# Kernel tuning notes

Hardware: AMD Instinct MI355X
Metric: run time of the kernel (lower is better)

The kernel has to match this reference:

```python
import jax, jax.numpy as jnp
import numpy as np
import math

B, L, LC = 2, 2048, 2048
D_MODEL, D_CROSS, D_HEAD = 1024, 1024, 64
N_HEADS = D_MODEL // D_HEAD
D6 = D_HEAD // 6  # freq bands per spatial axis (k-diffusion AxialRoPE, 3 axes)
EPS = 1e-6


def rope_freqs():
    n = N_HEADS * D6
    f = jnp.exp(jnp.linspace(math.log(math.pi), math.log(10.0 * math.pi), n + 1)[:-1])
    return f.reshape(D6, N_HEADS).T  # [nh, d6]


def rope_theta(pos):
    # pos: [b, l, 3] -> theta: [b, nh, l, 3*d6]
    f = rope_freqs()
    th = jnp.concatenate([pos[..., None, a:a + 1] * f for a in range(3)], axis=-1)  # [b,l,nh,3*d6]
    return jnp.moveaxis(th, -2, -3)


def apply_rotary(x, theta):
    d = theta.shape[-1]
    x1, x2, x3 = x[..., :d], x[..., d:2 * d], x[..., 2 * d:]
    c, s = jnp.cos(theta), jnp.sin(theta)
    return jnp.concatenate([x1 * c - x2 * s, x2 * c + x1 * s, x3], axis=-1)


def rms_norm(x, scale, eps=EPS):
    ms = jnp.mean(x * x, axis=-1, keepdims=True)
    return x * (scale * jax.lax.rsqrt(ms + eps))


def cosine_scale(q, k, scale, eps=EPS):
    s = jnp.sqrt(scale)[:, None, None]  # [nh,1,1]
    qn = q * (s * jax.lax.rsqrt(jnp.sum(q * q, axis=-1, keepdims=True) + eps))
    kn = k * (s * jax.lax.rsqrt(jnp.sum(k * k, axis=-1, keepdims=True) + eps))
    return qn, kn


def setup_inputs():
    key = jax.random.key(0)
    ks = jax.random.split(key, 8)
    return {
        "x": jax.random.normal(ks[0], (B, L, D_MODEL), jnp.float32),
        "pos": jax.random.uniform(ks[1], (B, L, 3), jnp.float32),
        "x_cross": jax.random.normal(ks[2], (B, LC, D_CROSS), jnp.float32),
        "pos_cross": jax.random.uniform(ks[3], (B, LC, 3), jnp.float32),
        "norm_scale": jnp.ones((D_MODEL,), jnp.float32),
        "norm_cross_scale": jnp.ones((D_CROSS,), jnp.float32),
        "q_w": jax.random.normal(ks[4], (D_MODEL, D_MODEL), jnp.float32) * 0.02,
        "kv_w": jax.random.normal(ks[5], (2 * D_MODEL, D_CROSS), jnp.float32) * 0.02,
        "head_scale": jnp.full((N_HEADS,), 10.0, jnp.float32),
        "out_w": jax.random.normal(ks[6], (D_MODEL, D_MODEL), jnp.float32) * 0.02,
    }


def reference(x, pos, x_cross, pos_cross, norm_scale, norm_cross_scale, q_w, kv_w, head_scale, out_w):
    skip = x
    xn = rms_norm(x, norm_scale)
    xc = rms_norm(x_cross, norm_cross_scale)
    q = xn @ q_w.T                       # [b,l,d]
    kv = xc @ kv_w.T                     # [b,lc,2d]
    b, l, _ = q.shape
    lc = kv.shape[1]
    q = q.reshape(b, l, N_HEADS, D_HEAD).transpose(0, 2, 1, 3)          # [b,nh,l,e]
    kv = kv.reshape(b, lc, 2, N_HEADS, D_HEAD)                          # (t nh e) factorization
    k = kv[:, :, 0].transpose(0, 2, 1, 3)
    v = kv[:, :, 1].transpose(0, 2, 1, 3)
    q, k = cosine_scale(q, k, head_scale)
    q = apply_rotary(q, rope_theta(pos))
    k = apply_rotary(k, rope_theta(pos_cross))
    attn = jax.nn.softmax(jnp.einsum('bhqe,bhke->bhqk', q, k), axis=-1)  # scale=1.0 (cosine-sim pre-scaled)
    o = jnp.einsum('bhqk,bhke->bhqe', attn, v)
    o = o.transpose(0, 2, 1, 3).reshape(b, l, D_MODEL)
    return o @ out_w.T + skip
```

## Files before the change

### kernel.cpp

```cpp
#include <hip/hip_runtime.h>

typedef __bf16 bf16_t;
typedef __bf16 bf16x4 __attribute__((ext_vector_type(4)));
typedef __bf16 bf16x8 __attribute__((ext_vector_type(8)));
typedef float f32x4 __attribute__((ext_vector_type(4)));
typedef short s16x4 __attribute__((ext_vector_type(4)));

#define B_DIM 2
#define L_DIM 2048
#define LC_DIM 2048
#define DM 1024
#define NH 16
#define DH 64
#define MB (1u << 20)
#define LOG2E 1.44269504088896f
#define NZ 2

__device__ __forceinline__ bool probe_is_f32(const unsigned* probe) {
  return probe[0] == 0x3F800000u;
}

__device__ __forceinline__ void async16(const bf16_t* g, bf16_t* l) {
  __builtin_amdgcn_global_load_lds((const __attribute__((address_space(1))) void*)g,
                                   (__attribute__((address_space(3))) void*)l, 16, 0, 0);
}

#if __has_builtin(__builtin_amdgcn_mfma_f32_16x16x16bf16_1k)
#define HAVE_K16 1
__device__ __forceinline__ f32x4 mfma16(bf16x4 a, bf16x4 b, f32x4 c) {
  union { bf16x4 h; s16x4 s; } ua, ub;
  ua.h = a; ub.h = b;
  return __builtin_amdgcn_mfma_f32_16x16x16bf16_1k(ua.s, ub.s, c, 0, 0, 0);
}
#else
#define HAVE_K16 0
#endif

__device__ __forceinline__ void conv_b(const void* src, bf16_t* dst, int i, bool f32) {
  bf16x4 w;
  if (f32) {
    f32x4 v = *(const f32x4*)((const float*)src + i);
    w[0] = (bf16_t)v[0]; w[1] = (bf16_t)v[1]; w[2] = (bf16_t)v[2]; w[3] = (bf16_t)v[3];
  } else {
    w = *(const bf16x4*)((const bf16_t*)src + i);
  }
  *(bf16x4*)(dst + i) = w;
}
__device__ __forceinline__ void conv_f(const void* src, float* dst, int i, int n, bool f32) {
  if (i >= n) return;
  f32x4 v;
  if (f32) {
    v = *(const f32x4*)((const float*)src + i);
  } else {
    bf16x4 w = *(const bf16x4*)((const bf16_t*)src + i);
    v[0] = (float)w[0]; v[1] = (float)w[1]; v[2] = (float)w[2]; v[3] = (float)w[3];
  }
  *(f32x4*)(dst + i) = v;
}

__global__ __launch_bounds__(256) void front_k(
    const void* x, const void* xc, const void* qw, const void* kvw, const void* ow,
    const void* pos, const void* posc, const void* ns, const void* ncs, const void* hs,
    bf16_t* xn, bf16_t* xcn, bf16_t* cqw, bf16_t* ckvw, bf16_t* cow,
    float* fpos, float* fposc, float* fns, float* fncs, float* fhs,
    const unsigned* probe) {
  const bool f32 = probe_is_f32(probe);
  const int tid = threadIdx.x;
  if (blockIdx.x < 2 * B_DIM * L_DIM) {
    const bool isB = blockIdx.x >= B_DIM * L_DIM;
    const int row = isB ? blockIdx.x - B_DIM * L_DIM : blockIdx.x;
    const void* src = isB ? xc : x;
    const void* scr = isB ? ncs : ns;
    bf16_t* out = isB ? xcn : xn;
    float f0, f1, f2, f3, s0, s1, s2, s3;
    if (f32) {
      f32x4 v = *((const f32x4*)((const float*)src + (size_t)row * DM) + tid);
      f0 = v[0]; f1 = v[1]; f2 = v[2]; f3 = v[3];
      f32x4 sv = *((const f32x4*)scr + tid);
      s0 = sv[0]; s1 = sv[1]; s2 = sv[2]; s3 = sv[3];
    } else {
      bf16x4 v = *((const bf16x4*)((const bf16_t*)src + (size_t)row * DM) + tid);
      f0 = (float)v[0]; f1 = (float)v[1]; f2 = (float)v[2]; f3 = (float)v[3];
      bf16x4 sv = *((const bf16x4*)scr + tid);
      s0 = (float)sv[0]; s1 = (float)sv[1]; s2 = (float)sv[2]; s3 = (float)sv[3];
    }
    float ss = f0 * f0 + f1 * f1 + f2 * f2 + f3 * f3;
#pragma unroll
    for (int m = 1; m < 64; m <<= 1) ss += __shfl_xor(ss, m, 64);
    __shared__ float red[4];
    const int wave = tid >> 6, lane = tid & 63;
    if (lane == 0) red[wave] = ss;
    __syncthreads();
    float ms = (red[0] + red[1] + red[2] + red[3]) * (1.0f / DM);
    float r = rsqrtf(ms + 1e-6f);
    bf16x4 w;
    w[0] = (bf16_t)(f0 * r * s0);
    w[1] = (bf16_t)(f1 * r * s1);
    w[2] = (bf16_t)(f2 * r * s2);
    w[3] = (bf16_t)(f3 * r * s3);
    *(bf16x4*)(out + (size_t)row * DM + tid * 4) = w;
    return;
  }
  const int blk = blockIdx.x - 2 * B_DIM * L_DIM;
  const int e4 = tid * 4;
  if (blk < 1024)       conv_b(qw,  cqw,  blk * 1024 + e4, f32);
  else if (blk < 3072)  conv_b(kvw, ckvw, (blk - 1024) * 1024 + e4, f32);
  else if (blk < 4096)  conv_b(ow,  cow,  (blk - 3072) * 1024 + e4, f32);
  else if (blk < 4108)  conv_f(pos,  fpos,  (blk - 4096) * 1024 + e4, 12288, f32);
  else if (blk < 4120)  conv_f(posc, fposc, (blk - 4108) * 1024 + e4, 12288, f32);
  else if (blk == 4120) conv_f(ns,  fns,  e4, 1024, f32);
  else if (blk == 4121) conv_f(ncs, fncs, e4, 1024, f32);
  else                  conv_f(hs,  fhs,  e4, 16, f32);
}

__global__ __launch_bounds__(256) void gemm_qkv_k(const bf16_t* __restrict__ xn,
                                                  const bf16_t* __restrict__ xcn,
                                                  const bf16_t* __restrict__ qw,
                                                  const bf16_t* __restrict__ kvw,
                                                  bf16_t* __restrict__ qb,
                                                  bf16_t* __restrict__ kvK,
                                                  bf16_t* __restrict__ Vp) {
  __shared__ bf16_t Asm[128 * 32];
  __shared__ bf16_t Wsm[128 * 32];
  const int tid = threadIdx.x;
  const int wave = tid >> 6, lane = tid & 63;
  const int quad = lane >> 4, tc = lane & 15;
  const int wr = wave >> 1, wc = wave & 1;
  const bool isq = blockIdx.y < 8;
  const bf16_t* A = isq ? xn : xcn;
  const bf16_t* W = isq ? qw : kvw;
  const int n0 = (isq ? blockIdx.y : (blockIdx.y - 8)) * 128;
  const int m0 = blockIdx.x * 128;
  const int K = 1024;

  const int srow = wave * 16 + (lane >> 2);
  const int scol = (lane & 3) * 8;
  const bf16_t* ag = A + (size_t)(m0 + srow) * K + scol;
  const bf16_t* wg = W + (size_t)(n0 + srow) * K + scol;
  bf16_t* al0 = &Asm[(wave * 16) * 32];
  bf16_t* al1 = &Asm[(64 + wave * 16) * 32];
  bf16_t* wl0 = &Wsm[(wave * 16) * 32];
  bf16_t* wl1 = &Wsm[(64 + wave * 16) * 32];

  f32x4 acc[4][4] = {};

  for (int k0 = 0; k0 < K; k0 += 32) {
    async16(ag + k0, al0);
    async16(ag + k0 + (size_t)64 * K, al1);
    async16(wg + k0, wl0);
    async16(wg + k0 + (size_t)64 * K, wl1);
    __syncthreads();
    bf16x8 af[4], wf[4];
#pragma unroll
    for (int i = 0; i < 4; ++i)
      af[i] = *(const bf16x8*)&Asm[(wr * 64 + i * 16 + tc) * 32 + quad * 8];
#pragma unroll
    for (int j = 0; j < 4; ++j)
      wf[j] = *(const bf16x8*)&Wsm[(wc * 64 + j * 16 + tc) * 32 + quad * 8];
#pragma unroll
    for (int i = 0; i < 4; ++i)
#pragma unroll
      for (int j = 0; j < 4; ++j)
        acc[i][j] = __builtin_amdgcn_mfma_f32_16x16x32_bf16(af[i], wf[j], acc[i][j], 0, 0, 0);
    __syncthreads();
  }

  if (isq || n0 < DM) {
    bf16_t* C = isq ? qb : kvK;
#pragma unroll
    for (int i = 0; i < 4; ++i) {
      const size_t row = (size_t)m0 + wr * 64 + i * 16 + quad * 4;
#pragma unroll
      for (int j = 0; j < 4; ++j) {
        const int col = n0 + wc * 64 + j * 16 + tc;
#pragma unroll
        for (int r = 0; r < 4; ++r)
          C[(row + r) * DM + col] = (bf16_t)acc[i][j][r];
      }
    }
  } else {
#pragma unroll
    for (int i = 0; i < 4; ++i) {
      const int row = m0 + wr * 64 + i * 16 + quad * 4;
      const int b = row >> 11, kc = row & (LC_DIM - 1);
#pragma unroll
      for (int j = 0; j < 4; ++j) {
        const int hd = n0 - DM + wc * 64 + j * 16 + tc;
        const int h = hd >> 6, d = hd & 63;
        bf16x4 pk;
        pk[0] = (bf16_t)acc[i][j][0];
        pk[1] = (bf16_t)acc[i][j][1];
        pk[2] = (bf16_t)acc[i][j][2];
        pk[3] = (bf16_t)acc[i][j][3];
        *(bf16x4*)(Vp + (((size_t)(b * NH + h) * (LC_DIM / 4) + (kc >> 2)) * DH + d) * 4) = pk;
      }
    }
  }
}

__global__ __launch_bounds__(256) void prep_k(bf16_t* __restrict__ q,
                                              const bf16_t* __restrict__ kvK,
                                              bf16_t* __restrict__ Kp,
                                              const float* __restrict__ pos,
                                              const float* __restrict__ pos_cross,
                                              const float* __restrict__ head_scale) {
  const int gw = (blockIdx.x * blockDim.x + threadIdx.x) >> 6;
  const int lane = threadIdx.x & 63;
  const int per = B_DIM * L_DIM * NH;
  const bool is_k = gw >= per;
  const int id = is_k ? gw - per : gw;
  const int h = id & 15;
  const int row = id >> 4;
  const bf16_t* src = (is_k ? kvK : q) + (size_t)row * DM + h * DH;
  const float* pp = (is_k ? pos_cross : pos) + (size_t)row * 3;

  float val = (float)src[lane];
  float ss = val * val;
#pragma unroll
  for (int m = 1; m < 64; m <<= 1) ss += __shfl_xor(ss, m, 64);
  float sc = sqrtf(head_scale[h]) * rsqrtf(ss + 1e-6f);
  if (!is_k) sc *= LOG2E;
  float vn = val * sc;

  const int j = lane;
  const int tj = j < 30 ? j : (j < 60 ? j - 30 : 0);
  const int a = tj >= 20 ? 2 : (tj >= 10 ? 1 : 0);
  const int jj = tj - a * 10;
  float p = pp[a];
  float freq = 3.14159265358979f *
               __builtin_amdgcn_exp2f((float)(jj * 16 + h) * 0.0207620505930f);
  float rev = p * freq * 0.15915494309189535f;
  rev -= floorf(rev);
  float cth = __builtin_amdgcn_cosf(rev);
  float sth = __builtin_amdgcn_sinf(rev);
  const int partner = j < 30 ? j + 30 : (j < 60 ? j - 30 : j);
  float vp = __shfl(vn, partner, 64);
  float outv;
  if (j < 30)       outv = vn * cth - vp * sth;
  else if (j < 60)  outv = vn * cth + vp * sth;
  else              outv = vn;

  if (is_k) {
    const int b = row >> 11, l = row & (LC_DIM - 1);
    Kp[(((size_t)b * NH + h) * LC_DIM + l) * DH + lane] = (bf16_t)outv;
  } else {
    q[(size_t)row * DM + h * DH + lane] = (bf16_t)outv;
  }
}

#define FLASH_LOAD(KB, VB, KC)                                                   \
  {                                                                              \
    _Pragma("unroll") for (int mt = 0; mt < 4; ++mt) {                           \
      _Pragma("unroll") for (int hf = 0; hf < 2; ++hf)                           \
        KB[mt][hf] = *(const bf16x8*)(kg + (size_t)((KC) + mt * 16 + tc) * DH +  \
                                      hf * 32 + quad * 8);                       \
      _Pragma("unroll") for (int dt = 0; dt < 4; ++dt)                           \
        VB[mt][dt] = *(const bf16x4*)(vp + ((size_t)(((KC) >> 2) + mt * 4 + quad) * DH + \
                                            dt * 16 + tc) * 4);                  \
    }                                                                            \
  }

#define FLASH_COMPUTE(KB, VB)                                                    \
  {                                                                              \
    _Pragma("unroll") for (int jj = 0; jj < 4; ++jj) {                           \
      f32x4 s[4];                                                                \
      _Pragma("unroll") for (int mt = 0; mt < 4; ++mt) {                         \
        f32x4 zf = {0.f, 0.f, 0.f, 0.f};                                         \
        zf = __builtin_amdgcn_mfma_f32_16x16x32_bf16(KB[mt][0], qf[jj][0], zf, 0, 0, 0); \
        zf = __builtin_amdgcn_mfma_f32_16x16x32_bf16(KB[mt][1], qf[jj][1], zf, 0, 0, 0); \
        s[mt] = zf;                                                              \
      }                                                                          \
      bf16x4 p[4];                                                               \
      _Pragma("unroll") for (int mt = 0; mt < 4; ++mt) {                         \
        p[mt][0] = (bf16_t)__builtin_amdgcn_exp2f(s[mt][0]);                     \
        p[mt][1] = (bf16_t)__builtin_amdgcn_exp2f(s[mt][1]);                     \
        p[mt][2] = (bf16_t)__builtin_amdgcn_exp2f(s[mt][2]);                     \
        p[mt][3] = (bf16_t)__builtin_amdgcn_exp2f(s[mt][3]);                     \
      }                                                                          \
      _Pragma("unroll") for (int mt = 0; mt < 4; ++mt) {                         \
        accL[jj] = mfma16(p[mt], ones, accL[jj]);                                \
        _Pragma("unroll") for (int dt = 0; dt < 4; ++dt)                         \
          accO[jj][dt] = mfma16(p[mt], VB[mt][dt], accO[jj][dt]);                \
      }                                                                          \
    }                                                                            \
  }

__global__ __launch_bounds__(64, 2) void flash12_k(const bf16_t* __restrict__ q,
                                                   const bf16_t* __restrict__ Kp,
                                                   const bf16_t* __restrict__ Vp,
                                                   bf16_t* __restrict__ Op,
                                                   float* __restrict__ lp) {
  const int lane = threadIdx.x;
  const int quad = lane >> 4, tc = lane & 15;
  const int bh = blockIdx.y, b = bh >> 4;
  const int z = blockIdx.z;
  const int q0 = blockIdx.x * 64;

  bf16x8 qf[4][2];
#pragma unroll
  for (int jj = 0; jj < 4; ++jj)
#pragma unroll
    for (int hf = 0; hf < 2; ++hf)
      qf[jj][hf] = *(const bf16x8*)(q + (size_t)(b * L_DIM + q0 + jj * 16 + tc) * DM +
                                    (bh & 15) * DH + hf * 32 + quad * 8);

  f32x4 accO[4][4] = {};
  const bf16_t* kg = Kp + (size_t)bh * LC_DIM * DH;
  const bf16_t* vp = Vp + (size_t)bh * (LC_DIM / 4) * DH * 4;
  const int base = z * 1024;

#if HAVE_K16
  f32x4 accL[4] = {};
  bf16x4 ones;
  ones[0] = (bf16_t)1.0f; ones[1] = (bf16_t)1.0f;
  ones[2] = (bf16_t)1.0f; ones[3] = (bf16_t)1.0f;

  bf16x8 k0f[4][2], k1f[4][2];
  bf16x4 v0f[4][4], v1f[4][4];
  FLASH_LOAD(k0f, v0f, base);
#pragma unroll 1
  for (int kc0 = base; kc0 < base + 1024; kc0 += 128) {
    FLASH_LOAD(k1f, v1f, kc0 + 64);
    FLASH_COMPUTE(k0f, v0f);
    if (kc0 + 128 < base + 1024) FLASH_LOAD(k0f, v0f, kc0 + 128);
    FLASH_COMPUTE(k1f, v1f);
  }
#else
  __shared__ bf16_t Psm[64 * 64];
  float lsum[4] = {0.f, 0.f, 0.f, 0.f};
  const int sw = tc & 7;
#pragma unroll 1
  for (int kc0 = base; kc0 < base + 1024; kc0 += 64) {
    bf16x8 kfr[4][2];
#pragma unroll
    for (int mt = 0; mt < 4; ++mt)
#pragma unroll
      for (int hf = 0; hf < 2; ++hf)
        kfr[mt][hf] = *(const bf16x8*)(kg + (size_t)(kc0 + mt * 16 + tc) * DH +
                                       hf * 32 + quad * 8);
#pragma unroll
    for (int jj = 0; jj < 4; ++jj) {
      f32x4 s[4];
#pragma unroll
      for (int mt = 0; mt < 4; ++mt) {
        f32x4 zf = {0.f, 0.f, 0.f, 0.f};
        zf = __builtin_amdgcn_mfma_f32_16x16x32_bf16(kfr[mt][0], qf[jj][0], zf, 0, 0, 0);
        zf = __builtin_amdgcn_mfma_f32_16x16x32_bf16(kfr[mt][1], qf[jj][1], zf, 0, 0, 0);
        s[mt] = zf;
      }
#pragma unroll
      for (int mt = 0; mt < 4; ++mt) {
        float p0 = __builtin_amdgcn_exp2f(s[mt][0]);
        float p1 = __builtin_amdgcn_exp2f(s[mt][1]);
        float p2 = __builtin_amdgcn_exp2f(s[mt][2]);
        float p3 = __builtin_amdgcn_exp2f(s[mt][3]);
        lsum[jj] += (p0 + p1) + (p2 + p3);
        bf16x4 pk;
        pk[0] = (bf16_t)p0; pk[1] = (bf16_t)p1; pk[2] = (bf16_t)p2; pk[3] = (bf16_t)p3;
        const int phys = (mt * 2 + (quad >> 1)) ^ sw;
        *(bf16x4*)&Psm[(jj * 16 + tc) * 64 + phys * 8 + (quad & 1) * 4] = pk;
      }
    }
#pragma unroll
    for (int kb = 0; kb < 2; ++kb) {
      bf16x8 vfull[4];
#pragma unroll
      for (int dt = 0; dt < 4; ++dt) {
        const size_t k4 = (size_t)((kc0 + kb * 32) >> 2) + quad * 2;
        bf16x4 lo = *(const bf16x4*)(vp + (k4 * DH + dt * 16 + tc) * 4);
        bf16x4 hi = *(const bf16x4*)(vp + ((k4 + 1) * DH + dt * 16 + tc) * 4);
#pragma unroll
        for (int e = 0; e < 4; ++e) { vfull[dt][e] = lo[e]; vfull[dt][4 + e] = hi[e]; }
      }
#pragma unroll
      for (int jp = 0; jp < 4; ++jp) {
        bf16x8 pf = *(const bf16x8*)&Psm[(jp * 16 + tc) * 64 + ((kb * 4 + quad) ^ sw) * 8];
#pragma unroll
        for (int dt = 0; dt < 4; ++dt)
          accO[jp][dt] = __builtin_amdgcn_mfma_f32_16x16x32_bf16(pf, vfull[dt], accO[jp][dt], 0, 0, 0);
      }
    }
  }
#endif

  bf16_t* Ob = Op + (size_t)(z * 32 + bh) * L_DIM * DH;
  float* lb = lp + (size_t)(z * 32 + bh) * L_DIM;
#if HAVE_K16
#pragma unroll
  for (int jj = 0; jj < 4; ++jj) {
    if (tc == 0) {
#pragma unroll
      for (int r = 0; r < 4; ++r) lb[q0 + jj * 16 + quad * 4 + r] = accL[jj][r];
    }
#pragma unroll
    for (int r = 0; r < 4; ++r) {
      const size_t qg = q0 + jj * 16 + quad * 4 + r;
#pragma unroll
      for (int dt = 0; dt < 4; ++dt)
        Ob[qg * DH + dt * 16 + tc] = (bf16_t)accO[jj][dt][r];
    }
  }
#else
#pragma unroll
  for (int jj = 0; jj < 4; ++jj) {
    lsum[jj] += __shfl_xor(lsum[jj], 16, 64);
    lsum[jj] += __shfl_xor(lsum[jj], 32, 64);
  }
#pragma unroll
  for (int jj = 0; jj < 4; ++jj) {
    if (quad == 0) lb[q0 + jj * 16 + tc] = lsum[jj];
#pragma unroll
    for (int r = 0; r < 4; ++r) {
      const size_t qg = q0 + jj * 16 + quad * 4 + r;
#pragma unroll
      for (int dt = 0; dt < 4; ++dt)
        Ob[qg * DH + dt * 16 + tc] = (bf16_t)accO[jj][dt][r];
    }
  }
#endif
}

__global__ __launch_bounds__(256) void gemm_out_k(const bf16_t* __restrict__ Op,
                                                  const float* __restrict__ lp,
                                                  const bf16_t* __restrict__ W,
                                                  const void* __restrict__ skip_raw,
                                                  void* __restrict__ out,
                                                  const unsigned* __restrict__ probe) {
  __shared__ bf16_t Asm[64 * 32];
  __shared__ bf16_t Wsm[128 * 32];
  const int tid = threadIdx.x;
  const int wave = tid >> 6, lane = tid & 63;
  const int quad = lane >> 4, tc = lane & 15;
  const int wr = wave >> 1, wc = wave & 1;
  const int m0 = blockIdx.x * 64, n0 = blockIdx.y * 128;
  const int K = 1024, N = 1024;

  const int srow = wave * 16 + (lane >> 2);
  const int scol = (lane & 3) * 8;
  const int arow = m0 + srow;
  const int bb = arow >> 11, l = arow & (L_DIM - 1);
  const size_t zoff = (size_t)32 * L_DIM * DH;
  const bf16_t* wg = W + (size_t)(n0 + srow) * K + scol;
  bf16_t* wl0 = &Wsm[(wave * 16) * 32];
  bf16_t* wl1 = &Wsm[(64 + wave * 16) * 32];

  f32x4 acc[2][4] = {};

  float lv0 = lp[(size_t)(bb * NH) * L_DIM + l];
  float lv1 = lp[(size_t)(32 + bb * NH) * L_DIM + l];
  bf16x8 a0 = *(const bf16x8*)(Op + ((size_t)(bb * NH) * L_DIM + l) * DH + scol);
  bf16x8 a1 = *(const bf16x8*)(Op + zoff + ((size_t)(bb * NH) * L_DIM + l) * DH + scol);

  for (int k0 = 0; k0 < K; k0 += 32) {
    async16(wg + k0, wl0);
    async16(wg + k0 + (size_t)64 * K, wl1);
    const float linv = 1.f / (lv0 + lv1);
    bf16x8 aw;
#pragma unroll
    for (int e = 0; e < 8; ++e)
      aw[e] = (bf16_t)(((float)a0[e] + (float)a1[e]) * linv);
    *(bf16x8*)&Asm[srow * 32 + scol] = aw;
    if (k0 + 32 < K) {
      const int kn = k0 + 32;
      const int bhn = bb * NH + (kn >> 6);
      if ((kn & 63) == 0) {
        lv0 = lp[(size_t)bhn * L_DIM + l];
        lv1 = lp[(size_t)(32 + bhn) * L_DIM + l];
      }
      const size_t obn = ((size_t)bhn * L_DIM + l) * DH + (kn & 63) + scol;
      a0 = *(const bf16x8*)(Op + obn);
      a1 = *(const bf16x8*)(Op + zoff + obn);
    }
    __syncthreads();
    bf16x8 af[2], wf[4];
#pragma unroll
    for (int i = 0; i < 2; ++i)
      af[i] = *(const bf16x8*)&Asm[(wr * 32 + i * 16 + tc) * 32 + quad * 8];
#pragma unroll
    for (int j = 0; j < 4; ++j)
      wf[j] = *(const bf16x8*)&Wsm[(wc * 64 + j * 16 + tc) * 32 + quad * 8];
#pragma unroll
    for (int i = 0; i < 2; ++i)
#pragma unroll
      for (int j = 0; j < 4; ++j)
        acc[i][j] = __builtin_amdgcn_mfma_f32_16x16x32_bf16(af[i], wf[j], acc[i][j], 0, 0, 0);
    __syncthreads();
  }

  const bool f32o = probe_is_f32(probe);
#pragma unroll
  for (int i = 0; i < 2; ++i) {
    const size_t row = (size_t)m0 + wr * 32 + i * 16 + quad * 4;
#pragma unroll
    for (int j = 0; j < 4; ++j) {
      const int col = n0 + wc * 64 + j * 16 + tc;
#pragma unroll
      for (int r = 0; r < 4; ++r) {
        const size_t idx = (row + r) * (size_t)N + col;
        float v = acc[i][j][r];
        if (f32o) {
          v += ((const float*)skip_raw)[idx];
          ((float*)out)[idx] = v;
        } else {
          v += (float)((const bf16_t*)skip_raw)[idx];
          ((bf16_t*)out)[idx] = (bf16_t)v;
        }
      }
    }
  }
}

extern "C" void kernel_launch(void* const* d_in, const int* in_sizes, int n_in,
                              void* d_out, int out_size, void* d_ws, size_t ws_size,
                              hipStream_t stream) {
  const unsigned* probe = (const unsigned*)d_in[4];
  char* ws = (char*)d_ws;

  bf16_t* cow  = (bf16_t*)(ws + 0 * MB);
  bf16_t* cqw  = (bf16_t*)(ws + 2 * MB);
  bf16_t* ckvw = (bf16_t*)(ws + 4 * MB);
  bf16_t* xn   = (bf16_t*)(ws + 8 * MB);
  bf16_t* xcn  = (bf16_t*)(ws + 16 * MB);
  bf16_t* Op   = (bf16_t*)(ws + 8 * MB);
  bf16_t* kvK  = (bf16_t*)(ws + 24 * MB);
  bf16_t* qb   = (bf16_t*)(ws + 32 * MB);
  bf16_t* Vp   = (bf16_t*)(ws + 40 * MB);
  bf16_t* Kp   = (bf16_t*)(ws + 48 * MB);
  float* lp    = (float*)(ws + 64 * MB);
  float* fpos  = (float*)(ws + 65 * MB);
  float* fposc = (float*)(ws + 65 * MB + 64 * 1024);
  float* fns   = (float*)(ws + 65 * MB + 128 * 1024);
  float* fncs  = (float*)(ws + 65 * MB + 144 * 1024);
  float* fhs   = (float*)(ws + 65 * MB + 160 * 1024);

  front_k<<<2 * B_DIM * L_DIM + 4123, 256, 0, stream>>>(
      d_in[0], d_in[2], d_in[6], d_in[7], d_in[9], d_in[1], d_in[3], d_in[4],
      d_in[5], d_in[8], xn, xcn, cqw, ckvw, cow, fpos, fposc, fns, fncs, fhs, probe);
  gemm_qkv_k<<<dim3(32, 24), 256, 0, stream>>>(xn, xcn, cqw, ckvw, qb, kvK, Vp);
  prep_k<<<(2 * B_DIM * L_DIM * NH) / 4, 256, 0, stream>>>(qb, kvK, Kp, fpos, fposc, fhs);
  flash12_k<<<dim3(L_DIM / 64, B_DIM * NH, NZ), 64, 0, stream>>>(qb, Kp, Vp, Op, lp);
  gemm_out_k<<<dim3(64, 8), 256, 0, stream>>>(Op, lp, cow, d_in[0], d_out, probe);
}
```

Measured before the change: 264.3 us.

## Stage K/V tiles in shared LDS across four waves with async double-buffering

Result: faster. 250.7 us (-5.2%).

```diff
diff --git a/kernel.cpp b/kernel.cpp
--- a/kernel.cpp
+++ b/kernel.cpp
@@ -15,6 +15,7 @@
 #define MB (1u << 20)
 #define LOG2E 1.44269504088896f
 #define NZ 2
+#define SPAN (LC_DIM / NZ)
 
 __device__ __forceinline__ bool probe_is_f32(const unsigned* probe) {
   return probe[0] == 0x3F800000u;
@@ -25,16 +26,15 @@
                                    (__attribute__((address_space(3))) void*)l, 16, 0, 0);
 }
 
+__device__ __forceinline__ f32x4 mfma16(bf16x4 a, bf16x4 b, f32x4 c) {
 #if __has_builtin(__builtin_amdgcn_mfma_f32_16x16x16bf16_1k)
-#define HAVE_K16 1
-__device__ __forceinline__ f32x4 mfma16(bf16x4 a, bf16x4 b, f32x4 c) {
   union { bf16x4 h; s16x4 s; } ua, ub;
   ua.h = a; ub.h = b;
   return __builtin_amdgcn_mfma_f32_16x16x16bf16_1k(ua.s, ub.s, c, 0, 0, 0);
-}
 #else
-#define HAVE_K16 0
+  return c;
 #endif
+}
 
 __device__ __forceinline__ void conv_b(const void* src, bf16_t* dst, int i, bool f32) {
   bf16x4 w;
@@ -242,182 +242,112 @@
 
   if (is_k) {
     const int b = row >> 11, l = row & (LC_DIM - 1);
-    Kp[(((size_t)b * NH + h) * LC_DIM + l) * DH + lane] = (bf16_t)outv;
+    const int dsw = (((lane >> 3) ^ (l & 7)) << 3) | (lane & 7);
+    Kp[(((size_t)b * NH + h) * LC_DIM + l) * DH + dsw] = (bf16_t)outv;
   } else {
     q[(size_t)row * DM + h * DH + lane] = (bf16_t)outv;
   }
 }
 
-#define FLASH_LOAD(KB, VB, KC)                                                   \
+#define STAGE13(BUF, KC)                                                         \
   {                                                                              \
+    const bf16_t* ks_ = kg + (size_t)(KC) * DH;                                  \
+    const bf16_t* vs_ = vg + (size_t)((KC) >> 2) * (DH * 4);                     \
+    const int so_ = wave * 1024 + lane * 8;                                      \
+    async16(ks_ + so_, &Kl[BUF][wave * 1024]);                                   \
+    async16(ks_ + so_ + 512, &Kl[BUF][wave * 1024 + 512]);                       \
+    async16(vs_ + so_, &Vl[BUF][wave * 1024]);                                   \
+    async16(vs_ + so_ + 512, &Vl[BUF][wave * 1024 + 512]);                       \
+  }
+
+#define COMPUTE13(BUF)                                                           \
+  {                                                                              \
+    bf16x8 KB[4][2];                                                             \
+    _Pragma("unroll") for (int mt = 0; mt < 4; ++mt)                             \
+      _Pragma("unroll") for (int hf = 0; hf < 2; ++hf)                           \
+        KB[mt][hf] = *(const bf16x8*)&Kl[BUF][(mt * 16 + tc) * 64 +              \
+                                              (((hf << 2) | quad) ^ (tc & 7)) * 8]; \
+    f32x4 s[4];                                                                  \
     _Pragma("unroll") for (int mt = 0; mt < 4; ++mt) {                           \
-      _Pragma("unroll") for (int hf = 0; hf < 2; ++hf)                           \
-        KB[mt][hf] = *(const bf16x8*)(kg + (size_t)((KC) + mt * 16 + tc) * DH +  \
-                                      hf * 32 + quad * 8);                       \
+      f32x4 zf = {0.f, 0.f, 0.f, 0.f};                                           \
+      zf = __builtin_amdgcn_mfma_f32_16x16x32_bf16(KB[mt][0], qf[0], zf, 0, 0, 0); \
+      zf = __builtin_amdgcn_mfma_f32_16x16x32_bf16(KB[mt][1], qf[1], zf, 0, 0, 0); \
+      s[mt] = zf;                                                                \
+    }                                                                            \
+    bf16x4 p[4];                                                                 \
+    _Pragma("unroll") for (int mt = 0; mt < 4; ++mt) {                           \
+      p[mt][0] = (bf16_t)__builtin_amdgcn_exp2f(s[mt][0]);                       \
+      p[mt][1] = (bf16_t)__builtin_amdgcn_exp2f(s[mt][1]);                       \
+      p[mt][2] = (bf16_t)__builtin_amdgcn_exp2f(s[mt][2]);                       \
+      p[mt][3] = (bf16_t)__builtin_amdgcn_exp2f(s[mt][3]);                       \
+    }                                                                            \
+    bf16x4 VB[4][4];                                                             \
+    _Pragma("unroll") for (int mt = 0; mt < 4; ++mt)                             \
       _Pragma("unroll") for (int dt = 0; dt < 4; ++dt)                           \
-        VB[mt][dt] = *(const bf16x4*)(vp + ((size_t)(((KC) >> 2) + mt * 4 + quad) * DH + \
-                                            dt * 16 + tc) * 4);                  \
+        VB[mt][dt] = *(const bf16x4*)&Vl[BUF][(mt * 4 + quad) * 256 +            \
+                                              (dt * 16 + tc) * 4];               \
+    _Pragma("unroll") for (int mt = 0; mt < 4; ++mt) {                           \
+      accL = mfma16(p[mt], ones, accL);                                          \
+      _Pragma("unroll") for (int dt = 0; dt < 4; ++dt)                           \
+        accO[dt] = mfma16(p[mt], VB[mt][dt], accO[dt]);                          \
     }                                                                            \
   }
 
-#define FLASH_COMPUTE(KB, VB)                                                    \
-  {                                                                              \
-    _Pragma("unroll") for (int jj = 0; jj < 4; ++jj) {                           \
-      f32x4 s[4];                                                                \
-      _Pragma("unroll") for (int mt = 0; mt < 4; ++mt) {                         \
-        f32x4 zf = {0.f, 0.f, 0.f, 0.f};                                         \
-        zf = __builtin_amdgcn_mfma_f32_16x16x32_bf16(KB[mt][0], qf[jj][0], zf, 0, 0, 0); \
-        zf = __builtin_amdgcn_mfma_f32_16x16x32_bf16(KB[mt][1], qf[jj][1], zf, 0, 0, 0); \
-        s[mt] = zf;                                                              \
-      }                                                                          \
-      bf16x4 p[4];                                                               \
-      _Pragma("unroll") for (int mt = 0; mt < 4; ++mt) {                         \
-        p[mt][0] = (bf16_t)__builtin_amdgcn_exp2f(s[mt][0]);                     \
-        p[mt][1] = (bf16_t)__builtin_amdgcn_exp2f(s[mt][1]);                     \
-        p[mt][2] = (bf16_t)__builtin_amdgcn_exp2f(s[mt][2]);                     \
-        p[mt][3] = (bf16_t)__builtin_amdgcn_exp2f(s[mt][3]);                     \
-      }                                                                          \
-      _Pragma("unroll") for (int mt = 0; mt < 4; ++mt) {                         \
-        accL[jj] = mfma16(p[mt], ones, accL[jj]);                                \
-        _Pragma("unroll") for (int dt = 0; dt < 4; ++dt)                         \
-          accO[jj][dt] = mfma16(p[mt], VB[mt][dt], accO[jj][dt]);                \
-      }                                                                          \
-    }                                                                            \
-  }
-
-__global__ __launch_bounds__(64, 2) void flash12_k(const bf16_t* __restrict__ q,
-                                                   const bf16_t* __restrict__ Kp,
-                                                   const bf16_t* __restrict__ Vp,
-                                                   bf16_t* __restrict__ Op,
-                                                   float* __restrict__ lp) {
-  const int lane = threadIdx.x;
+__global__ __launch_bounds__(256, 3) void flash13_k(const bf16_t* __restrict__ q,
+                                                    const bf16_t* __restrict__ Kp,
+                                                    const bf16_t* __restrict__ Vp,
+                                                    bf16_t* __restrict__ Op,
+                                                    float* __restrict__ lp) {
+  const int tid = threadIdx.x;
+  const int wave = tid >> 6, lane = tid & 63;
   const int quad = lane >> 4, tc = lane & 15;
   const int bh = blockIdx.y, b = bh >> 4;
   const int z = blockIdx.z;
-  const int q0 = blockIdx.x * 64;
-
-  bf16x8 qf[4][2];
-#pragma unroll
-  for (int jj = 0; jj < 4; ++jj)
-#pragma unroll
-    for (int hf = 0; hf < 2; ++hf)
-      qf[jj][hf] = *(const bf16x8*)(q + (size_t)(b * L_DIM + q0 + jj * 16 + tc) * DM +
-                                    (bh & 15) * DH + hf * 32 + quad * 8);
-
-  f32x4 accO[4][4] = {};
-  const bf16_t* kg = Kp + (size_t)bh * LC_DIM * DH;
-  const bf16_t* vp = Vp + (size_t)bh * (LC_DIM / 4) * DH * 4;
-  const int base = z * 1024;
-
-#if HAVE_K16
-  f32x4 accL[4] = {};
+  const int qr = blockIdx.x * 64 + wave * 16;
+
+  __shared__ bf16_t Kl[2][64 * 64];
+  __shared__ bf16_t Vl[2][64 * 64];
+
+  bf16x8 qf[2];
+#pragma unroll
+  for (int hf = 0; hf < 2; ++hf)
+    qf[hf] = *(const bf16x8*)(q + (size_t)(b * L_DIM + qr + tc) * DM +
+                              (bh & 15) * DH + hf * 32 + quad * 8);
+
+  f32x4 accO[4] = {};
+  f32x4 accL = {};
   bf16x4 ones;
   ones[0] = (bf16_t)1.0f; ones[1] = (bf16_t)1.0f;
   ones[2] = (bf16_t)1.0f; ones[3] = (bf16_t)1.0f;
 
-  bf16x8 k0f[4][2], k1f[4][2];
-  bf16x4 v0f[4][4], v1f[4][4];
-  FLASH_LOAD(k0f, v0f, base);
+  const bf16_t* kg = Kp + (size_t)bh * LC_DIM * DH;
+  const bf16_t* vg = Vp + (size_t)bh * (LC_DIM / 4) * DH * 4;
+  const int base = z * SPAN;
+
+  STAGE13(0, base);
+  __syncthreads();
+  int cur = 0;
 #pragma unroll 1
-  for (int kc0 = base; kc0 < base + 1024; kc0 += 128) {
-    FLASH_LOAD(k1f, v1f, kc0 + 64);
-    FLASH_COMPUTE(k0f, v0f);
-    if (kc0 + 128 < base + 1024) FLASH_LOAD(k0f, v0f, kc0 + 128);
-    FLASH_COMPUTE(k1f, v1f);
-  }
-#else
-  __shared__ bf16_t Psm[64 * 64];
-  float lsum[4] = {0.f, 0.f, 0.f, 0.f};
-  const int sw = tc & 7;
-#pragma unroll 1
-  for (int kc0 = base; kc0 < base + 1024; kc0 += 64) {
-    bf16x8 kfr[4][2];
-#pragma unroll
-    for (int mt = 0; mt < 4; ++mt)
-#pragma unroll
-      for (int hf = 0; hf < 2; ++hf)
-        kfr[mt][hf] = *(const bf16x8*)(kg + (size_t)(kc0 + mt * 16 + tc) * DH +
-                                       hf * 32 + quad * 8);
-#pragma unroll
-    for (int jj = 0; jj < 4; ++jj) {
-      f32x4 s[4];
-#pragma unroll
-      for (int mt = 0; mt < 4; ++mt) {
-        f32x4 zf = {0.f, 0.f, 0.f, 0.f};
-        zf = __builtin_amdgcn_mfma_f32_16x16x32_bf16(kfr[mt][0], qf[jj][0], zf, 0, 0, 0);
-        zf = __builtin_amdgcn_mfma_f32_16x16x32_bf16(kfr[mt][1], qf[jj][1], zf, 0, 0, 0);
-        s[mt] = zf;
-      }
-#pragma unroll
-      for (int mt = 0; mt < 4; ++mt) {
-        float p0 = __builtin_amdgcn_exp2f(s[mt][0]);
-        float p1 = __builtin_amdgcn_exp2f(s[mt][1]);
-        float p2 = __builtin_amdgcn_exp2f(s[mt][2]);
-        float p3 = __builtin_amdgcn_exp2f(s[mt][3]);
-        lsum[jj] += (p0 + p1) + (p2 + p3);
-        bf16x4 pk;
-        pk[0] = (bf16_t)p0; pk[1] = (bf16_t)p1; pk[2] = (bf16_t)p2; pk[3] = (bf16_t)p3;
-        const int phys = (mt * 2 + (quad >> 1)) ^ sw;
-        *(bf16x4*)&Psm[(jj * 16 + tc) * 64 + phys * 8 + (quad & 1) * 4] = pk;
-      }
-    }
-#pragma unroll
-    for (int kb = 0; kb < 2; ++kb) {
-      bf16x8 vfull[4];
-#pragma unroll
-      for (int dt = 0; dt < 4; ++dt) {
-        const size_t k4 = (size_t)((kc0 + kb * 32) >> 2) + quad * 2;
-        bf16x4 lo = *(const bf16x4*)(vp + (k4 * DH + dt * 16 + tc) * 4);
-        bf16x4 hi = *(const bf16x4*)(vp + ((k4 + 1) * DH + dt * 16 + tc) * 4);
-#pragma unroll
-        for (int e = 0; e < 4; ++e) { vfull[dt][e] = lo[e]; vfull[dt][4 + e] = hi[e]; }
-      }
-#pragma unroll
-      for (int jp = 0; jp < 4; ++jp) {
-        bf16x8 pf = *(const bf16x8*)&Psm[(jp * 16 + tc) * 64 + ((kb * 4 + quad) ^ sw) * 8];
-#pragma unroll
-        for (int dt = 0; dt < 4; ++dt)
-          accO[jp][dt] = __builtin_amdgcn_mfma_f32_16x16x32_bf16(pf, vfull[dt], accO[jp][dt], 0, 0, 0);
-      }
-    }
-  }
-#endif
+  for (int t = 0; t < SPAN / 64; ++t) {
+    if (t + 1 < SPAN / 64) STAGE13(cur ^ 1, base + (t + 1) * 64);
+    COMPUTE13(cur);
+    __syncthreads();
+    cur ^= 1;
+  }
 
   bf16_t* Ob = Op + (size_t)(z * 32 + bh) * L_DIM * DH;
   float* lb = lp + (size_t)(z * 32 + bh) * L_DIM;
-#if HAVE_K16
-#pragma unroll
-  for (int jj = 0; jj < 4; ++jj) {
-    if (tc == 0) {
-#pragma unroll
-      for (int r = 0; r < 4; ++r) lb[q0 + jj * 16 + quad * 4 + r] = accL[jj][r];
-    }
-#pragma unroll
-    for (int r = 0; r < 4; ++r) {
-      const size_t qg = q0 + jj * 16 + quad * 4 + r;
-#pragma unroll
-      for (int dt = 0; dt < 4; ++dt)
-        Ob[qg * DH + dt * 16 + tc] = (bf16_t)accO[jj][dt][r];
-    }
-  }
-#else
-#pragma unroll
-  for (int jj = 0; jj < 4; ++jj) {
-    lsum[jj] += __shfl_xor(lsum[jj], 16, 64);
-    lsum[jj] += __shfl_xor(lsum[jj], 32, 64);
-  }
-#pragma unroll
-  for (int jj = 0; jj < 4; ++jj) {
-    if (quad == 0) lb[q0 + jj * 16 + tc] = lsum[jj];
-#pragma unroll
-    for (int r = 0; r < 4; ++r) {
-      const size_t qg = q0 + jj * 16 + quad * 4 + r;
-#pragma unroll
-      for (int dt = 0; dt < 4; ++dt)
-        Ob[qg * DH + dt * 16 + tc] = (bf16_t)accO[jj][dt][r];
-    }
-  }
-#endif
+  if (tc == 0) {
+#pragma unroll
+    for (int r = 0; r < 4; ++r) lb[qr + quad * 4 + r] = accL[r];
+  }
+#pragma unroll
+  for (int r = 0; r < 4; ++r) {
+    const size_t qg = (size_t)qr + quad * 4 + r;
+#pragma unroll
+    for (int dt = 0; dt < 4; ++dt)
+      Ob[qg * DH + dt * 16 + tc] = (bf16_t)accO[dt][r];
+  }
 }
 
 __global__ __launch_bounds__(256) void gemm_out_k(const bf16_t* __restrict__ Op,
@@ -538,6 +468,6 @@
       d_in[5], d_in[8], xn, xcn, cqw, ckvw, cow, fpos, fposc, fns, fncs, fhs, probe);
   gemm_qkv_k<<<dim3(32, 24), 256, 0, stream>>>(xn, xcn, cqw, ckvw, qb, kvK, Vp);
   prep_k<<<(2 * B_DIM * L_DIM * NH) / 4, 256, 0, stream>>>(qb, kvK, Kp, fpos, fposc, fhs);
-  flash12_k<<<dim3(L_DIM / 64, B_DIM * NH, NZ), 64, 0, stream>>>(qb, Kp, Vp, Op, lp);
+  flash13_k<<<dim3(L_DIM / 64, B_DIM * NH, NZ), 256, 0, stream>>>(qb, Kp, Vp, Op, lp);
   gemm_out_k<<<dim3(64, 8), 256, 0, stream>>>(Op, lp, cow, d_in[0], d_out, probe);
 }
```
